# Kernel tuning notes

Hardware: AMD Instinct MI355X
Metric: run time of the kernel (lower is better)

Reference implementation:

```python
import jax, jax.numpy as jnp
import numpy as np
from math import sqrt

ALPHA = 1.0
EPS = 1e-8


def setup_inputs() -> dict:
    key = jax.random.key(0)
    k1, k2, k3 = jax.random.split(key, 3)
    B, L, S, H, E = 4, 2048, 2048, 16, 64
    queries = jax.random.normal(k1, (B, L, H, E), dtype=jnp.float32)
    keys = jax.random.normal(k2, (B, S, H, E), dtype=jnp.float32)
    values = jax.random.normal(k3, (B, S, H, E), dtype=jnp.float32)
    return {"queries": queries, "keys": keys, "values": values}


def reference(queries, keys, values):
    B, L, H, E = queries.shape
    scale = 1.0 / sqrt(E)
    # dot product scores: [B,H,L,S]
    dot = jnp.einsum('blhe,bshe->bhls', queries, keys)
    # squared norms: [B,H,L,1] and [B,H,1,S]
    qn2 = jnp.sum(queries * queries, axis=-1).transpose(0, 2, 1)[..., :, None]
    kn2 = jnp.sum(keys * keys, axis=-1).transpose(0, 2, 1)[..., None, :]
    # wedge (parallelogram area) norm^2 = |q|^2|k|^2 - (q.k)^2, clipped at 0
    wedge_norm = jnp.sqrt(jax.nn.relu(qn2 * kn2 - dot * dot) + EPS)
    scores = ((1.0 - ALPHA) * dot + ALPHA * wedge_norm) * scale
    A = jax.nn.softmax(scores, axis=-1)  # no mask (mask_flag=False), dropout=0
    V = jnp.einsum('bhls,bshd->blhd', A, values)
    return V, jnp.mean(jnp.abs(scores))
```

## Files before the change

kernel.cpp:

```cpp
#include <hip/hip_runtime.h>
#include <math.h>

constexpr int Bb = 4, Ll = 2048, Ss = 2048, Hh = 16, Ee = 64;
constexpr float S2E  = 0.125f * 1.44269504088896341f;
constexpr float EPS2 = 1e-8f * S2E * S2E;
constexpr float INV_CNT = 1.0f / (4.0f * 16.0f * 2048.0f * 2048.0f);
constexpr float SUM_SCALE = INV_CNT * 0.69314718055994531f;

typedef __attribute__((ext_vector_type(8))) short  short8;
typedef __attribute__((ext_vector_type(4))) float  floatx4;

#define MFMA __builtin_amdgcn_mfma_f32_16x16x32_bf16

#define GLL(gp, lp_)                                                       \
  __builtin_amdgcn_global_load_lds(                                        \
      (const __attribute__((address_space(1))) unsigned int*)(gp),         \
      (__attribute__((address_space(3))) unsigned int*)(lp_), 16, 0, 0)

__device__ __forceinline__ unsigned bfrnd(float f) {
  unsigned u = __builtin_bit_cast(unsigned, f);
  return u + 0x7fffu + ((u >> 16) & 1u);
}
__device__ __forceinline__ float sq4(float4 v) {
  return v.x * v.x + v.y * v.y + v.z * v.z + v.w * v.w;
}
__device__ __forceinline__ float4 mul4(float4 v, float s) {
  float4 r; r.x = v.x * s; r.y = v.y * s; r.z = v.z * s; r.w = v.w * s;
  return r;
}
__device__ __forceinline__ short8 pack8(float4 x, float4 y) {
  union { short8 s; unsigned u[4]; } r;
  r.u[0] = __builtin_amdgcn_perm(bfrnd(x.y), bfrnd(x.x), 0x07060302u);
  r.u[1] = __builtin_amdgcn_perm(bfrnd(x.w), bfrnd(x.z), 0x07060302u);
  r.u[2] = __builtin_amdgcn_perm(bfrnd(y.y), bfrnd(y.x), 0x07060302u);
  r.u[3] = __builtin_amdgcn_perm(bfrnd(y.w), bfrnd(y.z), 0x07060302u);
  return r.s;
}

__global__ __launch_bounds__(256) void geom_pre_kernel(
    const float* __restrict__ Kg, const float* __restrict__ Vg,
    short* __restrict__ Kbf, short* __restrict__ Vtg,
    float* __restrict__ kn2g, float* __restrict__ sumg) {
  const int tid = threadIdx.x, bid = blockIdx.x;
  const int st = bid & 31, h = (bid >> 5) & 15, b = bid >> 9;
  const int s0 = st * 64, bh = b * 16 + h;
  if (bid == 0 && tid == 0) *sumg = 0.0f;

  const int r64 = tid >> 2, ec = (tid & 3) * 16;
  const float4* kp = (const float4*)(Kg + (((size_t)b * Ss + s0 + r64) * Hh + h) * Ee + ec);
  float4 k0 = kp[0], k1 = kp[1], k2 = kp[2], k3 = kp[3];
  float kn = sq4(k0) + sq4(k1) + sq4(k2) + sq4(k3);
  kn += __shfl_xor(kn, 1);
  kn += __shfl_xor(kn, 2);
  if ((tid & 3) == 0) kn2g[(size_t)bh * Ss + s0 + r64] = kn;
  short* ko = Kbf + ((size_t)bh * Ss + s0 + r64) * Ee + ec;
  *(short8*)(ko)     = pack8(k0, k1);
  *(short8*)(ko + 8) = pack8(k2, k3);

  const int sq = tid >> 4, eq = tid & 15;
  const float* vb = Vg + (((size_t)b * Ss + s0 + sq * 4) * Hh + h) * Ee + eq * 4;
  float4 r0 = *(const float4*)(vb);
  float4 r1 = *(const float4*)(vb + Hh * Ee);
  float4 r2 = *(const float4*)(vb + 2 * Hh * Ee);
  float4 r3 = *(const float4*)(vb + 3 * Hh * Ee);
  short* vo = Vtg + ((size_t)bh * Ee + eq * 4) * Ss + s0 + sq * 4;
#pragma unroll
  for (int j = 0; j < 4; ++j) {
    uint2 t;
    t.x = __builtin_amdgcn_perm(bfrnd((&r1.x)[j]), bfrnd((&r0.x)[j]), 0x07060302u);
    t.y = __builtin_amdgcn_perm(bfrnd((&r3.x)[j]), bfrnd((&r2.x)[j]), 0x07060302u);
    *(uint2*)(vo + (size_t)j * Ss) = t;
  }
}

constexpr int KB0 = 0, VB0 = 8192, PB = 16384, KN2 = 24576;

__global__ __launch_bounds__(256, 4) void geom_attn_kernel(
    const float* __restrict__ Qg, const short* __restrict__ Kbf,
    const short* __restrict__ Vtg, const float* __restrict__ kn2g,
    float* __restrict__ outg, float* __restrict__ sumg) {
  __shared__ __align__(16) char smem[32768];

  const int tid = threadIdx.x, w = tid >> 6, lane = tid & 63;
  const int c = lane & 15, q4 = lane >> 4;
  const int bid = blockIdx.x;
  const int lt = bid & 15, h = (bid >> 4) & 15, b = bid >> 8;
  const int bh = b * 16 + h;
  const int l0 = lt * 128 + w * 32;

  short8 qb[2][2];
  float qn2v[2];
#pragma unroll
  for (int g = 0; g < 2; ++g) {
    const float4* qp = (const float4*)(Qg + (((size_t)b * Ll + l0 + g * 16 + c) * Hh + h) * Ee);
    float4 a0 = mul4(qp[2 * q4], S2E),     a1 = mul4(qp[2 * q4 + 1], S2E);
    float4 a2 = mul4(qp[8 + 2 * q4], S2E), a3 = mul4(qp[9 + 2 * q4], S2E);
    float qn = sq4(a0) + sq4(a1) + sq4(a2) + sq4(a3);
    qn += __shfl_xor(qn, 16);
    qn += __shfl_xor(qn, 32);
    qn2v[g] = qn;
    qb[g][0] = pack8(a0, a1);
    qb[g][1] = pack8(a2, a3);
  }

  const int rK = tid >> 3, pK = tid & 7;
  const char* kSrc = (const char*)Kbf + (size_t)bh * (Ss * 128) + rK * 128 + ((pK ^ (rK & 7)) * 16);
  const int eV = tid >> 2;
  const char* vSrc = (const char*)Vtg + (size_t)bh * (Ss * 128) + eV * (Ss * 2) + (((tid & 3) ^ (eV & 3)) * 16);
  char* kDstW = smem + KB0 + w * 1024;
  char* vDstW = smem + VB0 + w * 1024;

  {
    const char* knSrc = (const char*)kn2g + (size_t)bh * 8192 + (size_t)tid * 16;
    GLL(knSrc, smem + KN2 + w * 1024);
    GLL(knSrc + 4096, smem + KN2 + w * 1024 + 4096);
  }

  GLL(kSrc, kDstW);
  GLL(vSrc, vDstW);
  kSrc += 4096;
  vSrc += 64;

  floatx4 o[2][4] = {};
  float lp0 = 0.f, lp1 = 0.f, scsum = 0.f;

  const int kOff = c * 128 + ((q4 ^ (c & 7)) * 16);
  const int vOff = c * 64 + ((q4 ^ (c & 3)) * 16);
  const int pRd  = PB + w * 2048 + c * 64 + ((q4 ^ (c & 3)) * 16);
  const int pWrB = PB + w * 2048 + c * 64 + (q4 & 1) * 8;
  const int knRd = KN2 + q4 * 16;

  for (int it = 0; it < 64; ++it) {
    const int p = it & 1;
    __syncthreads();
    GLL(kSrc, kDstW + (p ^ 1) * 4096);
    GLL(vSrc, vDstW + (p ^ 1) * 4096);
    kSrc += 4096;
    vSrc += 64;

    const char* Kb = smem + KB0 + p * 4096;
    const char* Vb = smem + VB0 + p * 4096;

#pragma unroll
    for (int ct = 0; ct < 2; ++ct) {
      short8 ka0 = *(const short8*)(Kb + ct * 2048 + kOff);
      short8 ka1 = *(const short8*)(Kb + ct * 2048 + (kOff ^ 64));
      float4 knv = *(const float4*)(smem + knRd + it * 128 + ct * 64);
      const int pwCT = ((ct * 2 + (q4 >> 1)) ^ (c & 3)) * 16;
#pragma unroll
      for (int g = 0; g < 2; ++g) {
        floatx4 d = {0.f, 0.f, 0.f, 0.f};
        d = MFMA(ka0, qb[g][0], d, 0, 0, 0);
        d = MFMA(ka1, qb[g][1], d, 0, 0, 0);
        float pe[4];
#pragma unroll
        for (int r = 0; r < 4; ++r) {
          float dot = d[r];
          float w2 = fmaf(-dot, dot, qn2v[g] * (&knv.x)[r]);
          w2 = fmaxf(w2, EPS2);
          float rt = __builtin_amdgcn_sqrtf(w2);
          scsum += rt;
          float e = __builtin_amdgcn_exp2f(rt);
          if (g == 0) lp0 += e; else lp1 += e;
          pe[r] = e;
        }
        uint2 pk;
        pk.x = __builtin_amdgcn_perm(__builtin_bit_cast(unsigned, pe[1]),
                                     __builtin_bit_cast(unsigned, pe[0]), 0x07060302u);
        pk.y = __builtin_amdgcn_perm(__builtin_bit_cast(unsigned, pe[3]),
                                     __builtin_bit_cast(unsigned, pe[2]), 0x07060302u);
        *(uint2*)(smem + pWrB + g * 1024 + pwCT) = pk;
      }
    }

    short8 vb0 = *(const short8*)(Vb + vOff);
    short8 vb1 = *(const short8*)(Vb + 1024 + vOff);
    short8 vb2 = *(const short8*)(Vb + 2048 + vOff);
    short8 vb3 = *(const short8*)(Vb + 3072 + vOff);
#pragma unroll
    for (int g = 0; g < 2; ++g) {
      short8 pa = *(const short8*)(smem + pRd + g * 1024);
      o[g][0] = MFMA(pa, vb0, o[g][0], 0, 0, 0);
      o[g][1] = MFMA(pa, vb1, o[g][1], 0, 0, 0);
      o[g][2] = MFMA(pa, vb2, o[g][2], 0, 0, 0);
      o[g][3] = MFMA(pa, vb3, o[g][3], 0, 0, 0);
    }
  }

  __syncthreads();

  lp0 += __shfl_xor(lp0, 16); lp0 += __shfl_xor(lp0, 32);
  lp1 += __shfl_xor(lp1, 16); lp1 += __shfl_xor(lp1, 32);

#pragma unroll
  for (int g = 0; g < 2; ++g) {
    float lpg = (g == 0) ? lp0 : lp1;
#pragma unroll
    for (int r = 0; r < 4; ++r) {
      float inv = 1.0f / __shfl(lpg, q4 * 4 + r);
      float* orow = outg + (((size_t)b * Ll + l0 + g * 16 + q4 * 4 + r) * Hh + h) * Ee;
      orow[c]      = o[g][0][r] * inv;
      orow[16 + c] = o[g][1][r] * inv;
      orow[32 + c] = o[g][2][r] * inv;
      orow[48 + c] = o[g][3][r] * inv;
    }
  }

  scsum += __shfl_xor(scsum, 1);
  scsum += __shfl_xor(scsum, 2);
  scsum += __shfl_xor(scsum, 4);
  scsum += __shfl_xor(scsum, 8);
  scsum += __shfl_xor(scsum, 16);
  scsum += __shfl_xor(scsum, 32);
  if (lane == 0) atomicAdd(sumg, scsum * SUM_SCALE);
}

extern "C" void kernel_launch(void* const* d_in, const int* in_sizes, int n_in,
                              void* d_out, int out_size, void* d_ws, size_t ws_size,
                              hipStream_t stream) {
  const float* Q = (const float*)d_in[0];
  const float* K = (const float*)d_in[1];
  const float* V = (const float*)d_in[2];
  float* out   = (float*)d_out;
  float* sumsc = out + (size_t)Bb * Ll * Hh * Ee;

  short* Kbf = (short*)d_ws;
  short* Vtg = Kbf + (size_t)Bb * Hh * Ss * Ee;
  float* kn2 = (float*)(Vtg + (size_t)Bb * Hh * Ee * Ss);

  hipLaunchKernelGGL(geom_pre_kernel, dim3(Bb * Hh * (Ss / 64)), dim3(256), 0,
                     stream, K, V, Kbf, Vtg, kn2, sumsc);
  hipLaunchKernelGGL(geom_attn_kernel, dim3(Bb * Hh * (Ll / 128)), dim3(256), 0,
                     stream, Q, Kbf, Vtg, kn2, out, sumsc);
}
```

Before: 266.4 us.

## Keep probabilities in registers and feed PV via 16x16x16 MFMA, double key tile

The probability tile no longer round-trips through shared memory. The exponentiated scores stay in registers and feed directly as the B operand of 16x16x16 bf16 MFMAs, computing O^T = V^T P^T. The preprocess kernel writes V transposed in a pre-swizzled layout to match, the key tile per iteration doubles to 128 (32 iterations, larger LDS buffers), and output stores become float4. This removes the LDS writes and reads of P plus per-iteration sync pressure, at the cost of twice as many smaller MFMAs, more LDS per block (which may lower occupancy), and more register pressure.

```diff
diff --git a/kernel.cpp b/kernel.cpp
--- a/kernel.cpp
+++ b/kernel.cpp
@@ -8,9 +8,24 @@
 constexpr float SUM_SCALE = INV_CNT * 0.69314718055994531f;
 
 typedef __attribute__((ext_vector_type(8))) short  short8;
+typedef __attribute__((ext_vector_type(4))) short  short4v;
 typedef __attribute__((ext_vector_type(4))) float  floatx4;
 
-#define MFMA __builtin_amdgcn_mfma_f32_16x16x32_bf16
+#define MFMA32(A, B, C) __builtin_amdgcn_mfma_f32_16x16x32_bf16(A, B, C, 0, 0, 0)
+
+#if __has_builtin(__builtin_amdgcn_mfma_f32_16x16x16_bf16)
+#define MFMA16(A, B, C) __builtin_amdgcn_mfma_f32_16x16x16_bf16(A, B, C, 0, 0, 0)
+#elif __has_builtin(__builtin_amdgcn_mfma_f32_16x16x16bf16_1k)
+#define MFMA16(A, B, C) __builtin_amdgcn_mfma_f32_16x16x16bf16_1k(A, B, C, 0, 0, 0)
+#else
+static __device__ __forceinline__ floatx4 mfma16_asm(short4v a, short4v b, floatx4 c) {
+  floatx4 d;
+  asm volatile("v_mfma_f32_16x16x16_bf16 %0, %1, %2, %3"
+               : "=v"(d) : "v"(a), "v"(b), "v"(c));
+  return d;
+}
+#define MFMA16(A, B, C) mfma16_asm(A, B, C)
+#endif
 
 #define GLL(gp, lp_)                                                       \
   __builtin_amdgcn_global_load_lds(                                        \
@@ -39,7 +54,7 @@
 
 __global__ __launch_bounds__(256) void geom_pre_kernel(
     const float* __restrict__ Kg, const float* __restrict__ Vg,
-    short* __restrict__ Kbf, short* __restrict__ Vtg,
+    short* __restrict__ Kbf, char* __restrict__ Vtg,
     float* __restrict__ kn2g, float* __restrict__ sumg) {
   const int tid = threadIdx.x, bid = blockIdx.x;
   const int st = bid & 31, h = (bid >> 5) & 15, b = bid >> 9;
@@ -57,29 +72,34 @@
   *(short8*)(ko)     = pack8(k0, k1);
   *(short8*)(ko + 8) = pack8(k2, k3);
 
-  const int sq = tid >> 4, eq = tid & 15;
+  const int sq = tid >> 4;
+  const int eq = tid & 15;
   const float* vb = Vg + (((size_t)b * Ss + s0 + sq * 4) * Hh + h) * Ee + eq * 4;
   float4 r0 = *(const float4*)(vb);
   float4 r1 = *(const float4*)(vb + Hh * Ee);
   float4 r2 = *(const float4*)(vb + 2 * Hh * Ee);
   float4 r3 = *(const float4*)(vb + 3 * Hh * Ee);
-  short* vo = Vtg + ((size_t)bh * Ee + eq * 4) * Ss + s0 + sq * 4;
+  const int fsrc = ((sq >> 3) << 2) + (sq & 3);
+  const int half = (sq >> 2) & 1;
 #pragma unroll
   for (int j = 0; j < 4; ++j) {
+    const int d = eq * 4 + j;
+    const int pos = (fsrc + (d & 7)) & 7;
+    char* dst = Vtg + ((size_t)bh * 64 + d) * 4096 + st * 128 + pos * 16 + half * 8;
     uint2 t;
     t.x = __builtin_amdgcn_perm(bfrnd((&r1.x)[j]), bfrnd((&r0.x)[j]), 0x07060302u);
     t.y = __builtin_amdgcn_perm(bfrnd((&r3.x)[j]), bfrnd((&r2.x)[j]), 0x07060302u);
-    *(uint2*)(vo + (size_t)j * Ss) = t;
-  }
-}
-
-constexpr int KB0 = 0, VB0 = 8192, PB = 16384, KN2 = 24576;
+    *(uint2*)dst = t;
+  }
+}
+
+constexpr int KB0 = 0, VB0 = 16384, KN2 = 32768;
 
 __global__ __launch_bounds__(256, 4) void geom_attn_kernel(
-    const float* __restrict__ Qg, const short* __restrict__ Kbf,
-    const short* __restrict__ Vtg, const float* __restrict__ kn2g,
+    const float* __restrict__ Qg, const char* __restrict__ Kbf,
+    const char* __restrict__ Vtg, const float* __restrict__ kn2g,
     float* __restrict__ outg, float* __restrict__ sumg) {
-  __shared__ __align__(16) char smem[32768];
+  __shared__ __align__(16) char smem[40960];
 
   const int tid = threadIdx.x, w = tid >> 6, lane = tid & 63;
   const int c = lane & 15, q4 = lane >> 4;
@@ -103,55 +123,53 @@
     qb[g][1] = pack8(a2, a3);
   }
 
-  const int rK = tid >> 3, pK = tid & 7;
-  const char* kSrc = (const char*)Kbf + (size_t)bh * (Ss * 128) + rK * 128 + ((pK ^ (rK & 7)) * 16);
-  const int eV = tid >> 2;
-  const char* vSrc = (const char*)Vtg + (size_t)bh * (Ss * 128) + eV * (Ss * 2) + (((tid & 3) ^ (eV & 3)) * 16);
-  char* kDstW = smem + KB0 + w * 1024;
-  char* vDstW = smem + VB0 + w * 1024;
+  const int rr = tid >> 3, gk = ((tid & 7) ^ (rr & 7));
+  const char* kS = Kbf + (size_t)bh * (Ss * 128) + rr * 128 + gk * 16;
+  const char* vS = Vtg + (size_t)bh * (64 * 4096) + rr * 4096 + (tid & 7) * 16;
+  char* kD = smem + KB0 + w * 1024;
+  char* vD = smem + VB0 + w * 1024;
 
   {
-    const char* knSrc = (const char*)kn2g + (size_t)bh * 8192 + (size_t)tid * 16;
-    GLL(knSrc, smem + KN2 + w * 1024);
-    GLL(knSrc + 4096, smem + KN2 + w * 1024 + 4096);
-  }
-
-  GLL(kSrc, kDstW);
-  GLL(vSrc, vDstW);
-  kSrc += 4096;
-  vSrc += 64;
-
+    const char* knS = (const char*)kn2g + (size_t)bh * 8192 + w * 1024 + lane * 16;
+    GLL(knS, smem + KN2 + w * 1024);
+    GLL(knS + 4096, smem + KN2 + w * 1024 + 4096);
+  }
+  GLL(kS, kD);
+  GLL(kS + 4096, kD + 4096);
+  GLL(vS, vD);
+  GLL(vS + 131072, vD + 4096);
+  kS += 8192;
+  vS += 128;
+
+  const int kOff = c * 128 + ((q4 ^ (c & 7)) << 4);
+  const int vRow = c * 128;
   floatx4 o[2][4] = {};
   float lp0 = 0.f, lp1 = 0.f, scsum = 0.f;
 
-  const int kOff = c * 128 + ((q4 ^ (c & 7)) * 16);
-  const int vOff = c * 64 + ((q4 ^ (c & 3)) * 16);
-  const int pRd  = PB + w * 2048 + c * 64 + ((q4 ^ (c & 3)) * 16);
-  const int pWrB = PB + w * 2048 + c * 64 + (q4 & 1) * 8;
-  const int knRd = KN2 + q4 * 16;
-
-  for (int it = 0; it < 64; ++it) {
+  for (int it = 0; it < 32; ++it) {
     const int p = it & 1;
     __syncthreads();
-    GLL(kSrc, kDstW + (p ^ 1) * 4096);
-    GLL(vSrc, vDstW + (p ^ 1) * 4096);
-    kSrc += 4096;
-    vSrc += 64;
-
-    const char* Kb = smem + KB0 + p * 4096;
-    const char* Vb = smem + VB0 + p * 4096;
-
-#pragma unroll
-    for (int ct = 0; ct < 2; ++ct) {
+    GLL(kS, kD + (p ^ 1) * 8192);
+    GLL(kS + 4096, kD + (p ^ 1) * 8192 + 4096);
+    GLL(vS, vD + (p ^ 1) * 8192);
+    GLL(vS + 131072, vD + (p ^ 1) * 8192 + 4096);
+    kS += 8192;
+    vS += 128;
+
+    const char* Kb = smem + KB0 + p * 8192;
+    const char* Vb = smem + VB0 + p * 8192;
+
+    short4v pb[4][2];
+#pragma unroll
+    for (int ct = 0; ct < 4; ++ct) {
       short8 ka0 = *(const short8*)(Kb + ct * 2048 + kOff);
       short8 ka1 = *(const short8*)(Kb + ct * 2048 + (kOff ^ 64));
-      float4 knv = *(const float4*)(smem + knRd + it * 128 + ct * 64);
-      const int pwCT = ((ct * 2 + (q4 >> 1)) ^ (c & 3)) * 16;
+      float4 knv = *(const float4*)(smem + KN2 + it * 256 + ct * 64 + q4 * 16);
 #pragma unroll
       for (int g = 0; g < 2; ++g) {
         floatx4 d = {0.f, 0.f, 0.f, 0.f};
-        d = MFMA(ka0, qb[g][0], d, 0, 0, 0);
-        d = MFMA(ka1, qb[g][1], d, 0, 0, 0);
+        d = MFMA32(ka0, qb[g][0], d);
+        d = MFMA32(ka1, qb[g][1], d);
         float pe[4];
 #pragma unroll
         for (int r = 0; r < 4; ++r) {
@@ -169,24 +187,28 @@
                                      __builtin_bit_cast(unsigned, pe[0]), 0x07060302u);
         pk.y = __builtin_amdgcn_perm(__builtin_bit_cast(unsigned, pe[3]),
                                      __builtin_bit_cast(unsigned, pe[2]), 0x07060302u);
-        *(uint2*)(smem + pWrB + g * 1024 + pwCT) = pk;
+        pb[ct][g] = __builtin_bit_cast(short4v, pk);
       }
     }
 
-    short8 vb0 = *(const short8*)(Vb + vOff);
-    short8 vb1 = *(const short8*)(Vb + 1024 + vOff);
-    short8 vb2 = *(const short8*)(Vb + 2048 + vOff);
-    short8 vb3 = *(const short8*)(Vb + 3072 + vOff);
-#pragma unroll
-    for (int g = 0; g < 2; ++g) {
-      short8 pa = *(const short8*)(smem + pRd + g * 1024);
-      o[g][0] = MFMA(pa, vb0, o[g][0], 0, 0, 0);
-      o[g][1] = MFMA(pa, vb1, o[g][1], 0, 0, 0);
-      o[g][2] = MFMA(pa, vb2, o[g][2], 0, 0, 0);
-      o[g][3] = MFMA(pa, vb3, o[g][3], 0, 0, 0);
+#pragma unroll
+    for (int cp = 0; cp < 2; ++cp) {
+      const int gsel = (((cp << 2) + q4 + (c & 7)) & 7) << 4;
+#pragma unroll
+      for (int dt = 0; dt < 4; ++dt) {
+        short8 vv = *(const short8*)(Vb + dt * 2048 + vRow + gsel);
+        short4v va0 = __builtin_shufflevector(vv, vv, 0, 1, 2, 3);
+        short4v va1 = __builtin_shufflevector(vv, vv, 4, 5, 6, 7);
+#pragma unroll
+        for (int g = 0; g < 2; ++g) {
+          o[g][dt] = MFMA16(va0, pb[2 * cp][g], o[g][dt]);
+          o[g][dt] = MFMA16(va1, pb[2 * cp + 1][g], o[g][dt]);
+        }
+      }
     }
   }
 
+  __builtin_amdgcn_s_waitcnt(0);
   __syncthreads();
 
   lp0 += __shfl_xor(lp0, 16); lp0 += __shfl_xor(lp0, 32);
@@ -194,15 +216,16 @@
 
 #pragma unroll
   for (int g = 0; g < 2; ++g) {
-    float lpg = (g == 0) ? lp0 : lp1;
-#pragma unroll
-    for (int r = 0; r < 4; ++r) {
-      float inv = 1.0f / __shfl(lpg, q4 * 4 + r);
-      float* orow = outg + (((size_t)b * Ll + l0 + g * 16 + q4 * 4 + r) * Hh + h) * Ee;
-      orow[c]      = o[g][0][r] * inv;
-      orow[16 + c] = o[g][1][r] * inv;
-      orow[32 + c] = o[g][2][r] * inv;
-      orow[48 + c] = o[g][3][r] * inv;
+    float inv = 1.0f / (g == 0 ? lp0 : lp1);
+    float* orow = outg + (((size_t)b * Ll + l0 + g * 16 + c) * Hh + h) * Ee;
+#pragma unroll
+    for (int dt = 0; dt < 4; ++dt) {
+      float4 st;
+      st.x = o[g][dt][0] * inv;
+      st.y = o[g][dt][1] * inv;
+      st.z = o[g][dt][2] * inv;
+      st.w = o[g][dt][3] * inv;
+      *(float4*)(orow + dt * 16 + q4 * 4) = st;
     }
   }
 
@@ -225,11 +248,11 @@
   float* sumsc = out + (size_t)Bb * Ll * Hh * Ee;
 
   short* Kbf = (short*)d_ws;
-  short* Vtg = Kbf + (size_t)Bb * Hh * Ss * Ee;
-  float* kn2 = (float*)(Vtg + (size_t)Bb * Hh * Ee * Ss);
+  char*  Vtg = (char*)(Kbf + (size_t)Bb * Hh * Ss * Ee);
+  float* kn2 = (float*)(Vtg + (size_t)Bb * Hh * Ee * Ss * 2);
 
   hipLaunchKernelGGL(geom_pre_kernel, dim3(Bb * Hh * (Ss / 64)), dim3(256), 0,
                      stream, K, V, Kbf, Vtg, kn2, sumsc);
   hipLaunchKernelGGL(geom_attn_kernel, dim3(Bb * Hh * (Ll / 128)), dim3(256), 0,
-                     stream, Q, Kbf, Vtg, kn2, out, sumsc);
-}
+                     stream, Q, (const char*)Kbf, (const char*)Vtg, kn2, out, sumsc);
+}
```

After: 273.8 us. 2.8% more time.
